# Optimization experiments

Measured on AMD Instinct MI355X. Metric: run time of the kernel, lower is better.

The kernel has to match this reference:

```python
import jax, jax.numpy as jnp
import numpy as np

B, N, E, Q = 4, 10000, 160000, 256
D, M, U, H, P = 128, 64, 126, 128, 7  # node_dim, msg_sz, update_sz, mlp hidden, pose dim
MSG_STEPS = 3
NUM_COPIES = 1


def setup_inputs() -> dict:
    key = jax.random.key(0)
    ks = jax.random.split(key, 12)
    return {
        "nodes_states": jax.random.normal(ks[0], (B, N, D), jnp.float32),
        "query_poses": jax.random.normal(ks[1], (B, Q, P), jnp.float32),
        "attn": jax.random.uniform(ks[2], (B, Q, N), jnp.float32) / N,
        "edge_sources": jax.random.randint(ks[3], (E,), 0, N),
        "edge_sinks": jax.random.randint(ks[4], (E,), 0, N),
        "w1e": jax.random.normal(ks[5], (2 * D, H), jnp.float32) * 0.05,
        "b1e": jnp.zeros((H,), jnp.float32),
        "w2e": jax.random.normal(ks[6], (H, M), jnp.float32) * 0.05,
        "b2e": jnp.zeros((M,), jnp.float32),
        "w1n": jax.random.normal(ks[7], (D + M, H), jnp.float32) * 0.05,
        "b1n": jnp.zeros((H,), jnp.float32),
        "w2n": jax.random.normal(ks[8], (H, U), jnp.float32) * 0.05,
        "b2n": jnp.zeros((U,), jnp.float32),
    }


def reference(nodes_states, query_poses, attn, edge_sources, edge_sinks,
              w1e, b1e, w2e, b2e, w1n, b1n, w2n, b2n):
    def step(states, _):
        # gather endpoint states: [B, E, 2*D]
        einp = jnp.concatenate([states[:, edge_sources], states[:, edge_sinks]], axis=-1)
        # edge MLP -> per-edge messages [B, E, M]
        msg = jax.nn.relu(einp @ w1e + b1e) @ w2e + b2e
        # scatter-add messages to sink nodes [B, N, M]
        incoming = jnp.zeros((states.shape[0], N, M), states.dtype).at[:, edge_sinks].add(msg)
        # node MLP update [B, N, U]
        ninp = jnp.concatenate([incoming, states], axis=-1)
        upd = jax.nn.relu(ninp @ w1n + b1n) @ w2n + b2n
        # only the last U channels (state part, not positions) are updated
        states = states.at[:, :, -U:].add(upd)
        return states, None

    states, _ = jax.lax.scan(step, nodes_states, None, length=MSG_STEPS)
    extraction = jnp.einsum('bqn,bnd->bqd', attn, states)  # interpolation readout
    return jnp.concatenate([query_poses] * NUM_COPIES + [extraction], axis=-1)
```

## Files before the change

### kernel.cpp

```cpp
#include <hip/hip_runtime.h>

#define Bx 4
#define Nn 10000
#define Ee 160000
#define Qq 256
#define Dd 128
#define Mm 64
#define Uu 126
#define Hh 128
#define Pp 7

#define KG 1252

typedef unsigned short u16;
typedef __bf16 bf16x8 __attribute__((ext_vector_type(8)));
typedef float f32x4 __attribute__((ext_vector_type(4)));

__device__ __forceinline__ float b2f(u16 h){
  unsigned u = ((unsigned)h) << 16; float f; __builtin_memcpy(&f, &u, 4); return f;
}
__device__ __forceinline__ u16 f2b(float f){
  __bf16 h = (__bf16)f; u16 r; __builtin_memcpy(&r, &h, 2); return r;
}
__device__ __forceinline__ float ldin(const void* p, long i, int flag){
  return flag ? b2f(((const u16*)p)[i]) : ((const float*)p)[i];
}

__global__ void probe_kernel(const void* in0, int* flag){
  __shared__ int cnt;
  if (threadIdx.x == 0) cnt = 0;
  __syncthreads();
  float a = fabsf(b2f(((const u16*)in0)[threadIdx.x]));
  if (a > 0.0009765625f && a < 32.0f) atomicAdd(&cnt, 1);
  __syncthreads();
  if (threadIdx.x == 0) *flag = (cnt >= 240) ? 1 : 0;
}

__global__ void prep_init_kernel(const void* w1e, const void* b1e, const void* w2e, const void* b2e,
                                 const void* w1n, const void* b1n, const void* w2n, const void* b2n,
                                 const void* in0, const int* __restrict__ snk,
                                 const int* __restrict__ flag,
                                 u16* w1e_s, u16* w2e_s, u16* w1n_s, u16* w2n_s,
                                 float* b1e_f, float* b2e_f, float* b1n_f, float* b2n_f,
                                 float* __restrict__ sf, u16* __restrict__ sbm,
                                 int* __restrict__ cnt)
{
  int f = *flag;
  long gsz = (long)gridDim.x * blockDim.x;
  long base = (long)blockIdx.x * blockDim.x + threadIdx.x;
  for (long idx = base; idx < 82368; idx += gsz){
    if (idx < 32768){
      int k = (int)idx >> 7, h = (int)idx & 127;
      w1e_s[(k >> 3) * 1024 + h * 8 + (k & 7)] = f2b(ldin(w1e, idx, f));
    } else if (idx < 40960){
      int i2 = (int)idx - 32768; int k = i2 >> 6, m2 = i2 & 63;
      w2e_s[(k & 15) * 512 + m2 * 8 + (k >> 4)] = f2b(ldin(w2e, i2, f));
    } else if (idx < 65536){
      int i2 = (int)idx - 40960; int k = i2 >> 7, h = i2 & 127;
      w1n_s[(k >> 3) * 1024 + h * 8 + (k & 7)] = f2b(ldin(w1n, i2, f));
    } else if (idx < 81920){
      int i2 = (int)idx - 65536; int k = i2 >> 7, u = i2 & 127;
      float v = (u < 126) ? ldin(w2n, (long)k * 126 + u, f) : 0.f;
      w2n_s[(k >> 3) * 1024 + u * 8 + (k & 7)] = f2b(v);
    } else if (idx < 82048){ b1e_f[idx - 81920] = ldin(b1e, idx - 81920, f); }
    else if (idx < 82112){ b2e_f[idx - 82048] = ldin(b2e, idx - 82048, f); }
    else if (idx < 82240){ b1n_f[idx - 82112] = ldin(b1n, idx - 82112, f); }
    else { int j = (int)idx - 82240; b2n_f[j] = (j < 126) ? ldin(b2n, j, f) : 0.f; }
  }
  const long total = (long)Bx * Nn * Dd;
  for (long i = base; i < total; i += gsz){
    float v = ldin(in0, i, f);
    sf[i] = v; sbm[i] = f2b(v);
  }
  for (long i = base; i < Ee; i += gsz)
    atomicAdd(&cnt[snk[(int)i]], 1);
}

__global__ void scan_kernel(const int* __restrict__ cnt, int* __restrict__ rowp){
  __shared__ int tot[1024];
  int t = threadIdx.x;
  int base = t * 10;
  int local[10]; int s = 0;
  #pragma unroll
  for (int i = 0; i < 10; i++){
    int v = (base + i < Nn) ? cnt[base + i] : 0;
    local[i] = s; s += v;
  }
  tot[t] = s;
  __syncthreads();
  for (int o = 1; o < 1024; o <<= 1){
    int v = (t >= o) ? tot[t - o] : 0;
    __syncthreads();
    tot[t] += v;
    __syncthreads();
  }
  int prefix = (t == 0) ? 0 : tot[t - 1];
  #pragma unroll
  for (int i = 0; i < 10; i++)
    if (base + i < Nn) rowp[base + i] = prefix + local[i];
  if (t == 1023) rowp[Nn] = tot[1023];
}
__global__ void fill_kernel(const int* __restrict__ src, const int* __restrict__ snk,
                            const int* __restrict__ rowp, int* __restrict__ cnt,
                            int* __restrict__ psrc){
  int i = blockIdx.x * blockDim.x + threadIdx.x;
  if (i < Ee){
    int s = snk[i];
    int p = rowp[s] + atomicAdd(&cnt[s], 1);
    psrc[p] = src[i];
  }
}

__global__ __launch_bounds__(256) void xform_kernel(
  const u16* __restrict__ sbm, const u16* __restrict__ w1s,
  const float* __restrict__ b1f, u16* __restrict__ xab)
{
  __shared__ __align__(16) u16 w1h[16384];
  int tid = threadIdx.x;
  int b = (blockIdx.x & 7) >> 1;
  int nt = ((blockIdx.x >> 3) << 1) + (blockIdx.x & 1);
  if (nt >= 157) return;
  int n0 = nt * 64;
  int w = tid >> 6, lane = tid & 63, m = lane & 15, quad = lane >> 4;
  int n = n0 + w * 16 + m;
  int nld = n < Nn ? n : Nn - 1;
  const u16* srow = sbm + (((size_t)b * Nn + nld) << 7);

  bf16x8 a[4];
  #pragma unroll
  for (int lk = 0; lk < 4; lk++) a[lk] = *(const bf16x8*)(srow + lk * 32 + quad * 8);

  const f32x4 z4 = {0.f, 0.f, 0.f, 0.f};
  float bb[8];
  #pragma unroll
  for (int ct = 0; ct < 8; ct++) bb[ct] = b1f[ct * 16 + m];

  #pragma unroll
  for (int half = 0; half < 2; half++){
    __syncthreads();
    {
      const uint4* g = (const uint4*)(w1s + half * 16384);
      uint4* l = (uint4*)w1h;
      #pragma unroll
      for (int i = 0; i < 8; i++) l[tid + i * 256] = g[tid + i * 256];
    }
    __syncthreads();
    f32x4 acc[8];
    #pragma unroll
    for (int ct = 0; ct < 8; ct++) acc[ct] = z4;
    #pragma unroll
    for (int lk = 0; lk < 4; lk++){
      #pragma unroll
      for (int ct = 0; ct < 8; ct++){
        bf16x8 bv = *(const bf16x8*)(w1h + (((lk * 4 + quad) << 7) + ct * 16 + m) * 8);
        acc[ct] = __builtin_amdgcn_mfma_f32_16x16x32_bf16(a[lk], bv, acc[ct], 0, 0, 0);
      }
    }
    #pragma unroll
    for (int i = 0; i < 4; i++){
      int r = n0 + w * 16 + quad * 4 + i;
      if (r < Nn){
        union { u16 h[8]; uint4 v; } t;
        #pragma unroll
        for (int ct = 0; ct < 8; ct++)
          t.h[ct] = f2b(acc[ct][i] + ((half == 0) ? bb[ct] : 0.f));
        *(uint4*)(xab + ((size_t)b * Nn + r) * 256 + half * 128 + m * 8) = t.v;
      }
    }
  }
}

__global__ __launch_bounds__(256) void node_kernel(
  float* __restrict__ sf, u16* __restrict__ sbm, const u16* __restrict__ xab,
  const int* __restrict__ rowp, const int* __restrict__ psrc,
  const u16* __restrict__ w2es, const float* __restrict__ b2ef,
  const u16* __restrict__ w1s, const u16* __restrict__ w2s,
  const float* __restrict__ b1f, const float* __restrict__ b2f2,
  const u16* __restrict__ w1es, const float* __restrict__ b1ef,
  u16* __restrict__ xabn, u16* __restrict__ sswz, int mode)
{
  __shared__ __align__(16) u16 ninp[64 * 200];
  __shared__ __align__(16) u16 hsYt[64 * 136];
  int b = (blockIdx.x & 7) >> 1;
  int nt = ((blockIdx.x >> 3) << 1) + (blockIdx.x & 1);
  if (nt >= 157) return;
  int n0 = nt * 64;
  int tid = threadIdx.x;

  {
    int nl = tid >> 2, part = tid & 3;
    int n = n0 + nl;
    float acc[32];
    #pragma unroll
    for (int i = 0; i < 32; i++) acc[i] = 0.f;
    if (n < Nn){
      float xbf[32];
      {
        const u16* xp = xab + ((size_t)b * Nn + n) * 256 + 128 + part * 8;
        union { uint4 v; u16 h[8]; } q0, q1, q2, q3;
        q0.v = *(const uint4*)(xp);
        q1.v = *(const uint4*)(xp + 32);
        q2.v = *(const uint4*)(xp + 64);
        q3.v = *(const uint4*)(xp + 96);
        #pragma unroll
        for (int j = 0; j < 8; j++){
          xbf[j] = b2f(q0.h[j]); xbf[8 + j] = b2f(q1.h[j]);
          xbf[16 + j] = b2f(q2.h[j]); xbf[24 + j] = b2f(q3.h[j]);
        }
      }
      int r0 = rowp[n], r1 = rowp[n + 1];
      const u16* xb0 = xab + (size_t)b * Nn * 256 + part * 8;
      for (int r = r0; r < r1; r++){
        int s = psrc[r];
        const u16* xs = xb0 + (size_t)s * 256;
        union { uint4 v; u16 h[8]; } q0, q1, q2, q3;
        q0.v = *(const uint4*)(xs);
        q1.v = *(const uint4*)(xs + 32);
        q2.v = *(const uint4*)(xs + 64);
        q3.v = *(const uint4*)(xs + 96);
        #pragma unroll
        for (int j = 0; j < 8; j++){
          float v0 = b2f(q0.h[j]) + xbf[j];
          acc[j] += v0 > 0.f ? v0 : 0.f;
          float v1 = b2f(q1.h[j]) + xbf[8 + j];
          acc[8 + j] += v1 > 0.f ? v1 : 0.f;
          float v2 = b2f(q2.h[j]) + xbf[16 + j];
          acc[16 + j] += v2 > 0.f ? v2 : 0.f;
          float v3 = b2f(q3.h[j]) + xbf[24 + j];
          acc[24 + j] += v3 > 0.f ? v3 : 0.f;
        }
      }
    }
    union { u16 h[32]; uint4 v[4]; } hb;
    #pragma unroll
    for (int i = 0; i < 32; i++) hb.h[i] = f2b(acc[i]);
    u16* hp = hsYt + nl * 136 + part * 8;
    *(uint4*)(hp)      = hb.v[0];
    *(uint4*)(hp + 32) = hb.v[1];
    *(uint4*)(hp + 64) = hb.v[2];
    *(uint4*)(hp + 96) = hb.v[3];
    u16* dp = ninp + nl * 200 + 64 + part * 8;
    if (n < Nn){
      const u16* sp = sbm + (((size_t)b * Nn + n) << 7) + part * 8;
      *(uint4*)(dp)      = *(const uint4*)(sp);
      *(uint4*)(dp + 32) = *(const uint4*)(sp + 32);
      *(uint4*)(dp + 64) = *(const uint4*)(sp + 64);
      *(uint4*)(dp + 96) = *(const uint4*)(sp + 96);
    } else {
      uint4 zz = {0, 0, 0, 0};
      *(uint4*)(dp)      = zz;
      *(uint4*)(dp + 32) = zz;
      *(uint4*)(dp + 64) = zz;
      *(uint4*)(dp + 96) = zz;
    }
  }

  int w = tid >> 6, lane = tid & 63, m = lane & 15, quad = lane >> 4;
  const f32x4 z4 = {0.f, 0.f, 0.f, 0.f};

  {
    f32x4 acc[4];
    #pragma unroll
    for (int ct = 0; ct < 4; ct++) acc[ct] = z4;
    #pragma unroll
    for (int ks = 0; ks < 4; ks++){
      bf16x8 a = *(const bf16x8*)(hsYt + (w * 16 + m) * 136 + ks * 32 + quad * 8);
      #pragma unroll
      for (int ct = 0; ct < 4; ct++){
        bf16x8 bv = *(const bf16x8*)(w2es + (((ks * 4 + quad) << 6) + ct * 16 + m) * 8);
        acc[ct] = __builtin_amdgcn_mfma_f32_16x16x32_bf16(a, bv, acc[ct], 0, 0, 0);
      }
    }
    #pragma unroll
    for (int i = 0; i < 4; i++){
      int n = n0 + w * 16 + quad * 4 + i;
      float deg = (n < Nn) ? (float)(rowp[n + 1] - rowp[n]) : 0.f;
      #pragma unroll
      for (int ct = 0; ct < 4; ct++)
        ninp[(w * 16 + quad * 4 + i) * 200 + ct * 16 + m] = f2b(acc[ct][i] + deg * b2ef[ct * 16 + m]);
    }
  }

  f32x4 acc1[8];
  #pragma unroll
  for (int ct = 0; ct < 8; ct++) acc1[ct] = z4;
  #pragma unroll 1
  for (int ks = 0; ks < 6; ks++){
    bf16x8 a = *(const bf16x8*)(ninp + (w * 16 + m) * 200 + ks * 32 + quad * 8);
    #pragma unroll
    for (int ct = 0; ct < 8; ct++){
      bf16x8 bv = *(const bf16x8*)(w1s + (((ks * 4 + quad) << 7) + ct * 16 + m) * 8);
      acc1[ct] = __builtin_amdgcn_mfma_f32_16x16x32_bf16(a, bv, acc1[ct], 0, 0, 0);
    }
  }
  #pragma unroll
  for (int ct = 0; ct < 8; ct++){
    float bb = b1f[ct * 16 + m];
    #pragma unroll
    for (int i = 0; i < 4; i++){
      float v = acc1[ct][i] + bb;
      v = v > 0.f ? v : 0.f;
      hsYt[(w * 16 + quad * 4 + i) * 136 + ct * 16 + m] = f2b(v);
    }
  }
  f32x4 acc2[8];
  #pragma unroll
  for (int ct = 0; ct < 8; ct++) acc2[ct] = z4;
  #pragma unroll 1
  for (int ko = 0; ko < 4; ko++){
    bf16x8 a2 = *(const bf16x8*)(hsYt + (w * 16 + m) * 136 + ko * 32 + quad * 8);
    #pragma unroll
    for (int ct = 0; ct < 8; ct++){
      bf16x8 bv = *(const bf16x8*)(w2s + (((ko * 4 + quad) << 7) + ct * 16 + m) * 8);
      acc2[ct] = __builtin_amdgcn_mfma_f32_16x16x32_bf16(a2, bv, acc2[ct], 0, 0, 0);
    }
  }

  #pragma unroll
  for (int ct = 0; ct < 8; ct++){
    int u = ct * 16 + m;
    if (u < 126){
      float bb = b2f2[u];
      #pragma unroll
      for (int i = 0; i < 4; i++){
        int nl = w * 16 + quad * 4 + i;
        int n = n0 + nl;
        if (n < Nn){
          size_t idx = (((size_t)b * Nn + n) << 7) + 2 + u;
          float v = sf[idx] + acc2[ct][i] + bb;
          if (mode == 0){
            sf[idx] = v;
            sbm[idx] = f2b(v);
          }
          hsYt[nl * 136 + 2 + u] = f2b(v);
        } else {
          hsYt[nl * 136 + 2 + u] = 0;
        }
      }
    }
  }
  if (m < 2){
    #pragma unroll
    for (int i = 0; i < 4; i++){
      int nl = w * 16 + quad * 4 + i;
      hsYt[nl * 136 + m] = ninp[nl * 200 + 64 + m];
    }
  }

  if (mode == 0){
    #pragma unroll
    for (int half = 0; half < 2; half++){
      f32x4 xacc[8];
      #pragma unroll
      for (int ct = 0; ct < 8; ct++) xacc[ct] = z4;
      #pragma unroll
      for (int st = 0; st < 2; st++){
        __syncthreads();
        {
          const uint4* g = (const uint4*)(w1es + half * 16384 + st * 8192);
          uint4* l = (uint4*)ninp;
          #pragma unroll
          for (int i = 0; i < 4; i++) l[tid + i * 256] = g[tid + i * 256];
        }
        __syncthreads();
        #pragma unroll
        for (int lk = 0; lk < 2; lk++){
          bf16x8 a = *(const bf16x8*)(hsYt + (w * 16 + m) * 136 + st * 64 + lk * 32 + quad * 8);
          #pragma unroll
          for (int ct = 0; ct < 8; ct++){
            bf16x8 bv = *(const bf16x8*)(ninp + (((lk * 4 + quad) << 7) + ct * 16 + m) * 8);
            xacc[ct] = __builtin_amdgcn_mfma_f32_16x16x32_bf16(a, bv, xacc[ct], 0, 0, 0);
          }
        }
      }
      #pragma unroll
      for (int i = 0; i < 4; i++){
        int r = n0 + w * 16 + quad * 4 + i;
        if (r < Nn){
          union { u16 h[8]; uint4 v; } t;
          #pragma unroll
          for (int ct = 0; ct < 8; ct++)
            t.h[ct] = f2b(xacc[ct][i] + ((half == 0) ? b1ef[ct * 16 + m] : 0.f));
          *(uint4*)(xabn + ((size_t)b * Nn + r) * 256 + half * 128 + m * 8) = t.v;
        }
      }
    }
  } else {
    #pragma unroll
    for (int r = 0; r < 2; r++){
      int kg = nt * 8 + w * 2 + r;
      if (kg < KG){
        #pragma unroll
        for (int dd = 0; dd < 2; dd++){
          int d = dd * 64 + lane;
          union { u16 h[8]; uint4 v; } t;
          #pragma unroll
          for (int j = 0; j < 8; j++) t.h[j] = hsYt[(w * 16 + r * 8 + j) * 136 + d];
          *(uint4*)(sswz + (((size_t)b * KG + kg) * 128 + d) * 8) = t.v;
        }
      }
    }
  }
}

__global__ __launch_bounds__(256) void extract2_kernel(
  const void* __restrict__ attn, const int* __restrict__ flag,
  const u16* __restrict__ sswz, float* __restrict__ partsum)
{
  int f = *flag;
  int blk = blockIdx.x;
  int kc = blk & 31, qt = (blk >> 5) & 3, b = blk >> 7;
  int tid = threadIdx.x, w = tid >> 6, lane = tid & 63, m = lane & 15, quad = lane >> 4;
  int qr = qt * 4 + w, q0 = qr * 16;
  int kg0 = kc * 40;
  int nsteps = (kc == 31) ? 3 : 10;
  long arow = ((long)(b * Qq + q0 + m)) * Nn;
  const u16* ab16 = (const u16*)attn + arow;
  const float* af32 = (const float*)attn + arow;
  const u16* sbase = sswz + ((size_t)b) * KG * 1024;
  f32x4 acc[8];
  const f32x4 z4 = {0.f, 0.f, 0.f, 0.f};
  #pragma unroll
  for (int ct = 0; ct < 8; ct++) acc[ct] = z4;
  #pragma unroll 2
  for (int t = 0; t < nsteps; t++){
    int kg = kg0 + t * 4 + quad;
    int kgc = kg < KG ? kg : 0;
    bf16x8 a;
    if (kg < 1250){
      if (f){
        a = *(const bf16x8*)(ab16 + kg * 8);
      } else {
        const float* ap = af32 + kg * 8;
        float4 p0 = *(const float4*)ap;
        float4 p1 = *(const float4*)(ap + 4);
        a[0] = (__bf16)p0.x; a[1] = (__bf16)p0.y; a[2] = (__bf16)p0.z; a[3] = (__bf16)p0.w;
        a[4] = (__bf16)p1.x; a[5] = (__bf16)p1.y; a[6] = (__bf16)p1.z; a[7] = (__bf16)p1.w;
      }
    } else {
      #pragma unroll
      for (int j = 0; j < 8; j++) a[j] = (__bf16)0.f;
    }
    #pragma unroll
    for (int ct = 0; ct < 8; ct++){
      bf16x8 bv = *(const bf16x8*)(sbase + ((size_t)kgc * 128 + ct * 16 + m) * 8);
      acc[ct] = __builtin_amdgcn_mfma_f32_16x16x32_bf16(a, bv, acc[ct], 0, 0, 0);
    }
  }
  #pragma unroll
  for (int ct = 0; ct < 8; ct++){
    #pragma unroll
    for (int i = 0; i < 4; i++)
      atomicAdd(&partsum[(((size_t)b * Qq + q0 + quad * 4 + i) << 7) + ct * 16 + m], acc[ct][i]);
  }
}

__global__ void final_kernel(const void* __restrict__ poses, const int* __restrict__ flag,
                             const float* __restrict__ partsum, void* __restrict__ out)
{
  int f = *flag;
  const long total = (long)Bx * Qq * (Pp + Dd);
  for (long idx = (long)blockIdx.x * blockDim.x + threadIdx.x; idx < total; idx += (long)gridDim.x * blockDim.x){
    int j = (int)(idx % (Pp + Dd));
    long bq = idx / (Pp + Dd);
    float v;
    if (j < Pp){
      v = ldin(poses, bq * Pp + j, f);
    } else {
      v = partsum[(bq << 7) + (j - Pp)];
    }
    if (f) ((u16*)out)[idx] = f2b(v);
    else ((float*)out)[idx] = v;
  }
}

extern "C" void kernel_launch(void* const* d_in, const int* in_sizes, int n_in,
                              void* d_out, int out_size, void* d_ws, size_t ws_size,
                              hipStream_t stream)
{
  const void* in_states = d_in[0];
  const void* in_poses  = d_in[1];
  const void* in_attn   = d_in[2];
  const int*  in_src    = (const int*)d_in[3];
  const int*  in_snk    = (const int*)d_in[4];
  const void* in_w1e = d_in[5];  const void* in_b1e = d_in[6];
  const void* in_w2e = d_in[7];  const void* in_b2e = d_in[8];
  const void* in_w1n = d_in[9];  const void* in_b1n = d_in[10];
  const void* in_w2n = d_in[11]; const void* in_b2n = d_in[12];

  char* ws = (char*)d_ws;
  size_t off = 0;
  auto alloc = [&](size_t bytes){ size_t o = off; off = (off + bytes + 255) & ~(size_t)255; return o; };
  const size_t psumB = (size_t)Bx * Qq * Dd * 4;
  size_t o_sf   = alloc((size_t)Bx * Nn * Dd * 4);
  size_t o_sb   = alloc((size_t)Bx * Nn * Dd * 2);
  size_t o_xabA = alloc((size_t)Bx * Nn * 256 * 2);
  size_t o_xabB = alloc((size_t)Bx * Nn * 256 * 2);
  size_t o_rowp = alloc((size_t)(Nn + 1) * 4);
  size_t o_rcnt = alloc((size_t)Nn * 2 * 4 + psumB);
  size_t o_psrc = alloc((size_t)Ee * 4);
  size_t o_w1e  = alloc(32768 * 2);
  size_t o_w2e  = alloc(8192 * 2);
  size_t o_w1n  = alloc(24576 * 2);
  size_t o_w2n  = alloc(16384 * 2);
  size_t o_b1e  = alloc(128 * 4);
  size_t o_b2e  = alloc(64 * 4);
  size_t o_b1n  = alloc(128 * 4);
  size_t o_b2n  = alloc(128 * 4);
  size_t o_flag = alloc(4);
  size_t o_sswz = alloc((size_t)Bx * KG * 128 * 8 * 2);

  float* sf    = (float*)(ws + o_sf);
  u16*   sbm   = (u16*)(ws + o_sb);
  u16*   xabA  = (u16*)(ws + o_xabA);
  u16*   xabB  = (u16*)(ws + o_xabB);
  int*   rowp  = (int*)(ws + o_rowp);
  int*   rcnt  = (int*)(ws + o_rcnt);
  int*   rcnt2 = rcnt + Nn;
  float* psum  = (float*)(ws + o_rcnt + (size_t)Nn * 2 * 4);
  int*   psrc  = (int*)(ws + o_psrc);
  u16*   w1e_s = (u16*)(ws + o_w1e);
  u16*   w2e_s = (u16*)(ws + o_w2e);
  u16*   w1n_s = (u16*)(ws + o_w1n);
  u16*   w2n_s = (u16*)(ws + o_w2n);
  float* b1e_f = (float*)(ws + o_b1e);
  float* b2e_f = (float*)(ws + o_b2e);
  float* b1n_f = (float*)(ws + o_b1n);
  float* b2n_f = (float*)(ws + o_b2n);
  int*   flag  = (int*)(ws + o_flag);
  u16*   sswz  = (u16*)(ws + o_sswz);

  hipMemsetAsync(rcnt, 0, (size_t)Nn * 2 * 4 + psumB, stream);
  probe_kernel<<<1, 256, 0, stream>>>(in_states, flag);
  prep_init_kernel<<<1024, 256, 0, stream>>>(in_w1e, in_b1e, in_w2e, in_b2e,
                                             in_w1n, in_b1n, in_w2n, in_b2n,
                                             in_states, in_snk, flag,
                                             w1e_s, w2e_s, w1n_s, w2n_s,
                                             b1e_f, b2e_f, b1n_f, b2n_f,
                                             sf, sbm, rcnt);
  scan_kernel<<<1, 1024, 0, stream>>>(rcnt, rowp);
  fill_kernel<<<(Ee + 255) / 256, 256, 0, stream>>>(in_src, in_snk, rowp, rcnt2, psrc);

  xform_kernel<<<632, 256, 0, stream>>>(sbm, w1e_s, b1e_f, xabA);
  node_kernel<<<632, 256, 0, stream>>>(sf, sbm, xabA, rowp, psrc,
                                       w2e_s, b2e_f, w1n_s, w2n_s, b1n_f, b2n_f,
                                       w1e_s, b1e_f, xabB, sswz, 0);
  node_kernel<<<632, 256, 0, stream>>>(sf, sbm, xabB, rowp, psrc,
                                       w2e_s, b2e_f, w1n_s, w2n_s, b1n_f, b2n_f,
                                       w1e_s, b1e_f, xabA, sswz, 0);
  node_kernel<<<632, 256, 0, stream>>>(sf, sbm, xabA, rowp, psrc,
                                       w2e_s, b2e_f, w1n_s, w2n_s, b1n_f, b2n_f,
                                       w1e_s, b1e_f, xabB, sswz, 1);

  extract2_kernel<<<512, 256, 0, stream>>>(in_attn, flag, sswz, psum);
  final_kernel<<<540, 256, 0, stream>>>(in_poses, flag, psum, d_out);
}
```

Before: 340.0 us.

## Drop fp32 state copy, inline dtype probe, fuse CSR fill with first transform

Removes the fp32 master copy of node states, so residual updates now read the old value from the bf16 shared tile and write bf16 only. The separate probe kernel becomes a per-wave inline detection, and the CSR fill kernel is merged into the first edge-transform launch as extra blocks. State conversion is vectorised to 8 elements per thread. This cuts a large fp32 read/write stream and several launches, at the cost of accumulating residuals in bf16 across steps, which lowers precision.

```diff
diff --git a/kernel.cpp b/kernel.cpp
--- a/kernel.cpp
+++ b/kernel.cpp
@@ -26,26 +26,28 @@
   return flag ? b2f(((const u16*)p)[i]) : ((const float*)p)[i];
 }
 
-__global__ void probe_kernel(const void* in0, int* flag){
-  __shared__ int cnt;
-  if (threadIdx.x == 0) cnt = 0;
-  __syncthreads();
-  float a = fabsf(b2f(((const u16*)in0)[threadIdx.x]));
-  if (a > 0.0009765625f && a < 32.0f) atomicAdd(&cnt, 1);
-  __syncthreads();
-  if (threadIdx.x == 0) *flag = (cnt >= 240) ? 1 : 0;
+__device__ __forceinline__ int detect_flag(const void* in0){
+  int lane = threadIdx.x & 63;
+  const u16* p = (const u16*)in0;
+  int c = 0;
+  #pragma unroll
+  for (int j = 0; j < 4; j++){
+    float a = fabsf(b2f(p[lane * 4 + j]));
+    c += (a > 0.0009765625f && a < 32.0f) ? 1 : 0;
+  }
+  #pragma unroll
+  for (int o = 32; o; o >>= 1) c += __shfl_xor(c, o, 64);
+  return c >= 240;
 }
 
 __global__ void prep_init_kernel(const void* w1e, const void* b1e, const void* w2e, const void* b2e,
                                  const void* w1n, const void* b1n, const void* w2n, const void* b2n,
                                  const void* in0, const int* __restrict__ snk,
-                                 const int* __restrict__ flag,
                                  u16* w1e_s, u16* w2e_s, u16* w1n_s, u16* w2n_s,
                                  float* b1e_f, float* b2e_f, float* b1n_f, float* b2n_f,
-                                 float* __restrict__ sf, u16* __restrict__ sbm,
-                                 int* __restrict__ cnt)
+                                 u16* __restrict__ sbm, int* __restrict__ cnt)
 {
-  int f = *flag;
+  int f = detect_flag(in0);
   long gsz = (long)gridDim.x * blockDim.x;
   long base = (long)blockIdx.x * blockDim.x + threadIdx.x;
   for (long idx = base; idx < 82368; idx += gsz){
@@ -67,10 +69,19 @@
     else if (idx < 82240){ b1n_f[idx - 82112] = ldin(b1n, idx - 82112, f); }
     else { int j = (int)idx - 82240; b2n_f[j] = (j < 126) ? ldin(b2n, j, f) : 0.f; }
   }
-  const long total = (long)Bx * Nn * Dd;
-  for (long i = base; i < total; i += gsz){
-    float v = ldin(in0, i, f);
-    sf[i] = v; sbm[i] = f2b(v);
+  const long total8 = (long)Bx * Nn * Dd / 8;
+  for (long i = base; i < total8; i += gsz){
+    if (f){
+      *(uint4*)(sbm + i * 8) = *(const uint4*)((const u16*)in0 + i * 8);
+    } else {
+      const float* ip = (const float*)in0 + i * 8;
+      float4 a = *(const float4*)ip;
+      float4 b2 = *(const float4*)(ip + 4);
+      union { u16 h[8]; uint4 v; } t;
+      t.h[0] = f2b(a.x); t.h[1] = f2b(a.y); t.h[2] = f2b(a.z); t.h[3] = f2b(a.w);
+      t.h[4] = f2b(b2.x); t.h[5] = f2b(b2.y); t.h[6] = f2b(b2.z); t.h[7] = f2b(b2.w);
+      *(uint4*)(sbm + i * 8) = t.v;
+    }
   }
   for (long i = base; i < Ee; i += gsz)
     atomicAdd(&cnt[snk[(int)i]], 1);
@@ -100,25 +111,25 @@
     if (base + i < Nn) rowp[base + i] = prefix + local[i];
   if (t == 1023) rowp[Nn] = tot[1023];
 }
-__global__ void fill_kernel(const int* __restrict__ src, const int* __restrict__ snk,
-                            const int* __restrict__ rowp, int* __restrict__ cnt,
-                            int* __restrict__ psrc){
-  int i = blockIdx.x * blockDim.x + threadIdx.x;
-  if (i < Ee){
-    int s = snk[i];
-    int p = rowp[s] + atomicAdd(&cnt[s], 1);
-    psrc[p] = src[i];
-  }
-}
-
-__global__ __launch_bounds__(256) void xform_kernel(
+
+__global__ __launch_bounds__(256) void fill_xform_kernel(
+  const int* __restrict__ src, const int* __restrict__ snk,
+  const int* __restrict__ rowp, int* __restrict__ cnt, int* __restrict__ psrc,
   const u16* __restrict__ sbm, const u16* __restrict__ w1s,
   const float* __restrict__ b1f, u16* __restrict__ xab)
 {
   __shared__ __align__(16) u16 w1h[16384];
   int tid = threadIdx.x;
-  int b = (blockIdx.x & 7) >> 1;
-  int nt = ((blockIdx.x >> 3) << 1) + (blockIdx.x & 1);
+  if (blockIdx.x < 625){
+    int i = blockIdx.x * 256 + tid;
+    int s = snk[i];
+    int p = rowp[s] + atomicAdd(&cnt[s], 1);
+    psrc[p] = src[i];
+    return;
+  }
+  int xbid = blockIdx.x - 625;
+  int b = (xbid & 7) >> 1;
+  int nt = ((xbid >> 3) << 1) + (xbid & 1);
   if (nt >= 157) return;
   int n0 = nt * 64;
   int w = tid >> 6, lane = tid & 63, m = lane & 15, quad = lane >> 4;
@@ -171,7 +182,7 @@
 }
 
 __global__ __launch_bounds__(256) void node_kernel(
-  float* __restrict__ sf, u16* __restrict__ sbm, const u16* __restrict__ xab,
+  u16* __restrict__ sbm, const u16* __restrict__ xab,
   const int* __restrict__ rowp, const int* __restrict__ psrc,
   const u16* __restrict__ w2es, const float* __restrict__ b2ef,
   const u16* __restrict__ w1s, const u16* __restrict__ w2s,
@@ -326,13 +337,12 @@
         int nl = w * 16 + quad * 4 + i;
         int n = n0 + nl;
         if (n < Nn){
-          size_t idx = (((size_t)b * Nn + n) << 7) + 2 + u;
-          float v = sf[idx] + acc2[ct][i] + bb;
-          if (mode == 0){
-            sf[idx] = v;
-            sbm[idx] = f2b(v);
-          }
-          hsYt[nl * 136 + 2 + u] = f2b(v);
+          float old = b2f(ninp[nl * 200 + 64 + 2 + u]);
+          float v = old + acc2[ct][i] + bb;
+          u16 hv = f2b(v);
+          if (mode == 0)
+            sbm[(((size_t)b * Nn + n) << 7) + 2 + u] = hv;
+          hsYt[nl * 136 + 2 + u] = hv;
         } else {
           hsYt[nl * 136 + 2 + u] = 0;
         }
@@ -404,10 +414,10 @@
 }
 
 __global__ __launch_bounds__(256) void extract2_kernel(
-  const void* __restrict__ attn, const int* __restrict__ flag,
+  const void* __restrict__ attn, const void* __restrict__ in_states,
   const u16* __restrict__ sswz, float* __restrict__ partsum)
 {
-  int f = *flag;
+  int f = detect_flag(in_states);
   int blk = blockIdx.x;
   int kc = blk & 31, qt = (blk >> 5) & 3, b = blk >> 7;
   int tid = threadIdx.x, w = tid >> 6, lane = tid & 63, m = lane & 15, quad = lane >> 4;
@@ -455,10 +465,10 @@
   }
 }
 
-__global__ void final_kernel(const void* __restrict__ poses, const int* __restrict__ flag,
+__global__ void final_kernel(const void* __restrict__ poses, const void* __restrict__ in_states,
                              const float* __restrict__ partsum, void* __restrict__ out)
 {
-  int f = *flag;
+  int f = detect_flag(in_states);
   const long total = (long)Bx * Qq * (Pp + Dd);
   for (long idx = (long)blockIdx.x * blockDim.x + threadIdx.x; idx < total; idx += (long)gridDim.x * blockDim.x){
     int j = (int)(idx % (Pp + Dd));
@@ -492,7 +502,6 @@
   size_t off = 0;
   auto alloc = [&](size_t bytes){ size_t o = off; off = (off + bytes + 255) & ~(size_t)255; return o; };
   const size_t psumB = (size_t)Bx * Qq * Dd * 4;
-  size_t o_sf   = alloc((size_t)Bx * Nn * Dd * 4);
   size_t o_sb   = alloc((size_t)Bx * Nn * Dd * 2);
   size_t o_xabA = alloc((size_t)Bx * Nn * 256 * 2);
   size_t o_xabB = alloc((size_t)Bx * Nn * 256 * 2);
@@ -507,10 +516,8 @@
   size_t o_b2e  = alloc(64 * 4);
   size_t o_b1n  = alloc(128 * 4);
   size_t o_b2n  = alloc(128 * 4);
-  size_t o_flag = alloc(4);
   size_t o_sswz = alloc((size_t)Bx * KG * 128 * 8 * 2);
 
-  float* sf    = (float*)(ws + o_sf);
   u16*   sbm   = (u16*)(ws + o_sb);
   u16*   xabA  = (u16*)(ws + o_xabA);
   u16*   xabB  = (u16*)(ws + o_xabB);
@@ -527,31 +534,29 @@
   float* b2e_f = (float*)(ws + o_b2e);
   float* b1n_f = (float*)(ws + o_b1n);
   float* b2n_f = (float*)(ws + o_b2n);
-  int*   flag  = (int*)(ws + o_flag);
   u16*   sswz  = (u16*)(ws + o_sswz);
 
   hipMemsetAsync(rcnt, 0, (size_t)Nn * 2 * 4 + psumB, stream);
-  probe_kernel<<<1, 256, 0, stream>>>(in_states, flag);
   prep_init_kernel<<<1024, 256, 0, stream>>>(in_w1e, in_b1e, in_w2e, in_b2e,
                                              in_w1n, in_b1n, in_w2n, in_b2n,
-                                             in_states, in_snk, flag,
+                                             in_states, in_snk,
                                              w1e_s, w2e_s, w1n_s, w2n_s,
                                              b1e_f, b2e_f, b1n_f, b2n_f,
-                                             sf, sbm, rcnt);
+                                             sbm, rcnt);
   scan_kernel<<<1, 1024, 0, stream>>>(rcnt, rowp);
-  fill_kernel<<<(Ee + 255) / 256, 256, 0, stream>>>(in_src, in_snk, rowp, rcnt2, psrc);
-
-  xform_kernel<<<632, 256, 0, stream>>>(sbm, w1e_s, b1e_f, xabA);
-  node_kernel<<<632, 256, 0, stream>>>(sf, sbm, xabA, rowp, psrc,
+  fill_xform_kernel<<<1257, 256, 0, stream>>>(in_src, in_snk, rowp, rcnt2, psrc,
+                                              sbm, w1e_s, b1e_f, xabA);
+
+  node_kernel<<<632, 256, 0, stream>>>(sbm, xabA, rowp, psrc,
                                        w2e_s, b2e_f, w1n_s, w2n_s, b1n_f, b2n_f,
                                        w1e_s, b1e_f, xabB, sswz, 0);
-  node_kernel<<<632, 256, 0, stream>>>(sf, sbm, xabB, rowp, psrc,
+  node_kernel<<<632, 256, 0, stream>>>(sbm, xabB, rowp, psrc,
                                        w2e_s, b2e_f, w1n_s, w2n_s, b1n_f, b2n_f,
                                        w1e_s, b1e_f, xabA, sswz, 0);
-  node_kernel<<<632, 256, 0, stream>>>(sf, sbm, xabA, rowp, psrc,
+  node_kernel<<<632, 256, 0, stream>>>(sbm, xabA, rowp, psrc,
                                        w2e_s, b2e_f, w1n_s, w2n_s, b1n_f, b2n_f,
                                        w1e_s, b1e_f, xabB, sswz, 1);
 
-  extract2_kernel<<<512, 256, 0, stream>>>(in_attn, flag, sswz, psum);
-  final_kernel<<<540, 256, 0, stream>>>(in_poses, flag, psum, d_out);
-}
+  extract2_kernel<<<512, 256, 0, stream>>>(in_attn, in_states, sswz, psum);
+  final_kernel<<<540, 256, 0, stream>>>(in_poses, in_states, psum, d_out);
+}
```

After: 302.0 us (median of 2 runs). 1.13x faster.
